# Optimization experiments

Measured on AMD Instinct MI355X. Metric: run time of the kernel, lower is better.

## Reference

```python
import jax, jax.numpy as jnp
import numpy as np


def _unfold(x, k, pad, stride):
    # torch.nn.functional.unfold: [B,C,H,W] -> [B, C*k*k, L]
    B, C, H, W = x.shape
    xp = jnp.pad(x, ((0, 0), (0, 0), (pad, pad), (pad, pad)))
    Ho = (H + 2 * pad - k) // stride + 1
    Wo = (W + 2 * pad - k) // stride + 1
    ih = stride * jnp.arange(Ho)[:, None] + jnp.arange(k)[None, :]  # [Ho,k]
    iw = stride * jnp.arange(Wo)[:, None] + jnp.arange(k)[None, :]  # [Wo,k]
    p = xp[:, :, ih][:, :, :, :, iw]          # [B,C,Ho,k,Wo,k]
    p = p.transpose(0, 1, 3, 5, 2, 4)          # [B,C,k,k,Ho,Wo]
    return p.reshape(B, C * k * k, Ho * Wo)


def _fold(cols, out_hw, k, pad, stride):
    # torch.nn.functional.fold (col2im, overlap-add)
    B, D, L = cols.shape
    C = D // (k * k)
    Ho = (out_hw[0] + 2 * pad - k) // stride + 1
    Wo = (out_hw[1] + 2 * pad - k) // stride + 1
    x = cols.reshape(B, C, k, k, Ho, Wo).transpose(0, 1, 2, 4, 3, 5)  # [B,C,k,Ho,k,Wo]
    ih = stride * jnp.arange(Ho)[None, :] + jnp.arange(k)[:, None]    # [k,Ho]
    iw = stride * jnp.arange(Wo)[None, :] + jnp.arange(k)[:, None]    # [k,Wo]
    out = jnp.zeros((B, C, out_hw[0] + 2 * pad, out_hw[1] + 2 * pad), cols.dtype)
    out = out.at[:, :, ih[:, :, None, None], iw[None, None, :, :]].add(x)
    return out[:, :, pad:pad + out_hw[0], pad:pad + out_hw[1]]


def _l2norm(x, axis):
    # torch F.normalize with eps=1e-12 (clamp_min on the norm)
    n = jnp.sqrt(jnp.sum(x * x, axis=axis, keepdims=True))
    return x / jnp.clip(n, 1e-12)


def _cubic(x):
    # PyTorch bicubic kernel, a=-0.75
    a = -0.75
    ax = jnp.abs(x)
    ax2 = ax * ax
    ax3 = ax2 * ax
    w1 = (a + 2.0) * ax3 - (a + 3.0) * ax2 + 1.0
    w2 = a * ax3 - 5.0 * a * ax2 + 8.0 * a * ax - 4.0 * a
    return jnp.where(ax <= 1.0, w1, jnp.where(ax < 2.0, w2, 0.0))


def _upsample1d_bicubic(x, axis, scale):
    # align_corners=False: src = (dst+0.5)/scale - 0.5, border-replicated 4-tap
    n = x.shape[axis]
    out = jnp.arange(n * scale, dtype=jnp.float32)
    src = (out + 0.5) / scale - 0.5
    f = jnp.floor(src)
    t = src - f
    offs = jnp.arange(-1, 3)
    idx = jnp.clip(f[:, None].astype(jnp.int32) + offs[None, :], 0, n - 1)   # [No,4]
    w = _cubic(t[:, None] - offs[None, :].astype(jnp.float32))               # [No,4]
    g = jnp.take(x, idx, axis=axis)  # inserts dims (No,4) at `axis`
    w_shape = [1] * g.ndim
    w_shape[axis] = idx.shape[0]
    w_shape[axis + 1] = 4
    return jnp.sum(g * w.reshape(w_shape), axis=axis + 1)


def _bicubic(R, scale):
    # R: [B, N_ref, N_lr] treated as a 1-channel image, upscale both axes
    R = _upsample1d_bicubic(R, 1, scale)
    return _upsample1d_bicubic(R, 2, scale)


def setup_inputs() -> dict:
    key = jax.random.key(0)
    ks = jax.random.split(key, 9)
    shapes = {
        'lrsr_lv1': (2, 256, 16, 16), 'lrsr_lv2': (2, 128, 32, 32), 'lrsr_lv3': (2, 64, 64, 64),
        'refsr_lv1': (2, 256, 16, 16), 'refsr_lv2': (2, 128, 32, 32), 'refsr_lv3': (2, 64, 64, 64),
        'ref_lv1': (2, 64, 256, 256), 'ref_lv2': (2, 128, 128, 128), 'ref_lv3': (2, 256, 64, 64),
    }
    return {name: jax.random.normal(k, shp, dtype=jnp.float32)
            for k, (name, shp) in zip(ks, shapes.items())}


def reference(lrsr_lv1, lrsr_lv2, lrsr_lv3, refsr_lv1, refsr_lv2, refsr_lv3, ref_lv1, ref_lv2, ref_lv3):
    # unfold + L2-normalize descriptors
    l3 = _l2norm(_unfold(lrsr_lv3, 3, 1, 1), 1)   # [B, D3, N3]
    l2 = _l2norm(_unfold(lrsr_lv2, 3, 1, 1), 1)
    l1 = _l2norm(_unfold(lrsr_lv1, 3, 1, 1), 1)
    r3 = _l2norm(jnp.swapaxes(_unfold(refsr_lv3, 3, 1, 1), 1, 2), 2)  # [B, N3, D3]
    r2 = _l2norm(jnp.swapaxes(_unfold(refsr_lv2, 3, 1, 1), 1, 2), 2)
    r1 = _l2norm(jnp.swapaxes(_unfold(refsr_lv1, 3, 1, 1), 1, 2), 2)
    # cosine correlation per scale
    R3 = jnp.einsum('bnd,bdm->bnm', r3, l3)   # [B, N3, N3]
    R2 = jnp.einsum('bnd,bdm->bnm', r2, l2)   # [B, N3/4, N3/4]
    R1 = jnp.einsum('bnd,bdm->bnm', r1, l1)   # [B, N3/16, N3/16]
    R = (R3 + _bicubic(R2, 4) + _bicubic(R1, 16)) / 3.0
    star = jnp.max(R, axis=1)                 # [B, N3]
    arg = jnp.argmax(R, axis=1)               # [B, N3]
    # retrieval gather on reference patches
    u3 = _unfold(ref_lv3, 3, 1, 1)
    u2 = _unfold(ref_lv2, 6, 2, 2)
    u1 = _unfold(ref_lv1, 12, 4, 4)
    gather = lambda u: jnp.take_along_axis(u, arg[:, None, :], axis=2)
    B = lrsr_lv3.shape[0]
    H, W = lrsr_lv3.shape[2], lrsr_lv3.shape[3]
    T_lv3 = _fold(gather(u3), (H, W), 3, 1, 1) / 9.0
    T_lv2 = _fold(gather(u2), (2 * H, 2 * W), 6, 2, 2) / 9.0
    T_lv1 = _fold(gather(u1), (4 * H, 4 * W), 12, 4, 4) / 9.0
    S_3 = star.reshape(B, 1, H, W)
    return (S_3, T_lv3, T_lv2, T_lv1)
```

## Files before the change

### kernel.cpp

```cpp
#include <hip/hip_runtime.h>
#include <cstdint>

#define DIVUP(a,b) (((a)+(b)-1)/(b))

typedef __attribute__((ext_vector_type(4))) float f32x4;
typedef __attribute__((ext_vector_type(8))) _Float16 half8;

__device__ __forceinline__ void gload_lds16(const void* g, void* l) {
  __builtin_amdgcn_global_load_lds(
      (const __attribute__((address_space(1))) void*)g,
      (__attribute__((address_space(3))) void*)l, 16, 0, 0);
}

__device__ __forceinline__ float cubicw(float x) {
  float ax = fabsf(x);
  float ax2 = ax * ax;
  float ax3 = ax2 * ax;
  if (ax <= 1.0f) return 1.25f * ax3 - 2.25f * ax2 + 1.0f;
  if (ax < 2.0f)  return -0.75f * ax3 + 3.75f * ax2 - 6.0f * ax + 3.0f;
  return 0.0f;
}

__global__ void sumsq_multi(const float* __restrict__ r3, const float* __restrict__ l3,
                            const float* __restrict__ r2, const float* __restrict__ l2,
                            const float* __restrict__ r1, const float* __restrict__ l1,
                            float* __restrict__ S) {
  int blk = blockIdx.x;
  const float* x; int C, HW, so, base;
  if (blk < 32)      { x = r3; C = 64;  HW = 4096; so = 0;     base = 0;  }
  else if (blk < 64) { x = l3; C = 64;  HW = 4096; so = 8192;  base = 32; }
  else if (blk < 72) { x = r2; C = 128; HW = 1024; so = 16384; base = 64; }
  else if (blk < 80) { x = l2; C = 128; HW = 1024; so = 18432; base = 72; }
  else if (blk < 82) { x = r1; C = 256; HW = 256;  so = 20480; base = 80; }
  else               { x = l1; C = 256; HW = 256;  so = 20992; base = 82; }
  int i = (blk - base) * 256 + threadIdx.x;
  if (i >= 2 * HW) return;
  int pix = i % HW, b = i / HW;
  const float* p = x + (size_t)b * C * HW + pix;
  float s = 0.f;
  for (int c = 0; c < C; ++c) { float v = p[(size_t)c * HW]; s += v * v; }
  S[so + i] = s;
}

__global__ void invnorm_multi(const float* __restrict__ S, float* __restrict__ invn) {
  int blk = blockIdx.x;
  int H, so, base;
  if (blk < 32)      { H = 64; so = 0;     base = 0;  }
  else if (blk < 64) { H = 64; so = 8192;  base = 32; }
  else if (blk < 72) { H = 32; so = 16384; base = 64; }
  else if (blk < 80) { H = 32; so = 18432; base = 72; }
  else if (blk < 82) { H = 16; so = 20480; base = 80; }
  else               { H = 16; so = 20992; base = 82; }
  int W = H;
  int i = (blk - base) * 256 + threadIdx.x;
  if (i >= 2 * H * W) return;
  int p = i % (H * W), b = i / (H * W);
  int ph = p / W, pw = p % W;
  const float* Sb = S + so + (size_t)b * H * W;
  float s = 0.f;
  for (int ki = 0; ki < 3; ++ki) {
    int y = ph + ki - 1;
    if (y < 0 || y >= H) continue;
    for (int kj = 0; kj < 3; ++kj) {
      int xx = pw + kj - 1;
      if (xx < 0 || xx >= W) continue;
      s += Sb[y * W + xx];
    }
  }
  float n = fmaxf(sqrtf(s), 1e-12f);
  invn[so + i] = 1.0f / n;
}

__global__ void desc_split_multi(const float* __restrict__ r3, const float* __restrict__ l3,
                                 const float* __restrict__ r2, const float* __restrict__ l2,
                                 _Float16* __restrict__ r3hi, _Float16* __restrict__ r3lo,
                                 _Float16* __restrict__ l3hi, _Float16* __restrict__ l3lo,
                                 _Float16* __restrict__ r2hi, _Float16* __restrict__ r2lo,
                                 _Float16* __restrict__ l2hi, _Float16* __restrict__ l2lo,
                                 const float* __restrict__ invn) {
  int blk = blockIdx.x;
  const float* x; _Float16* hi; _Float16* lo; int C, H, io, base;
  if (blk < 2048)      { x = r3; hi = r3hi; lo = r3lo; C = 64;  H = 64; io = 0;     base = 0; }
  else if (blk < 4096) { x = l3; hi = l3hi; lo = l3lo; C = 64;  H = 64; io = 8192;  base = 2048; }
  else if (blk < 5120) { x = r2; hi = r2hi; lo = r2lo; C = 128; H = 32; io = 16384; base = 4096; }
  else                 { x = l2; hi = l2hi; lo = l2lo; C = 128; H = 32; io = 18432; base = 5120; }
  int W = H, HW = H * W;
  int i = (blk - base) * 256 + threadIdx.x;
  if (i >= 2 * C * HW) return;
  int c = i % C;
  int p = (i / C) % HW;
  int b = i / (C * HW);
  int ph = p / W, pw = p % W;
  float s = invn[io + b * HW + p];
  size_t obase = ((size_t)b * HW + p) * (size_t)(C * 9) + (size_t)c * 9;
  const float* xb = x + (size_t)(b * C + c) * HW;
#pragma unroll
  for (int r = 0; r < 9; ++r) {
    int y = ph + r / 3 - 1, xx = pw + r % 3 - 1;
    float v = 0.f;
    if (y >= 0 && y < H && xx >= 0 && xx < W) v = xb[y * W + xx] * s;
    _Float16 h = (_Float16)v;
    float hf = (float)h;
    _Float16 l = (_Float16)((v - hf) * 4096.0f);
    hi[obase + r] = h;
    lo[obase + r] = l;
  }
}

__global__ void desc_l1_kernel(const float* __restrict__ x, float* __restrict__ out,
                               const float* __restrict__ invn) {
  const int C = 256, H = 16, W = 16, HW = 256, D = 2304, io = 20992;
  int i = blockIdx.x * 256 + threadIdx.x;
  if (i >= 2 * D * HW) return;
  int p = i % HW;
  int d = (i / HW) % D;
  int b = i / (HW * D);
  int c = d / 9, r = d % 9, ki = r / 3, kj = r % 3;
  int ph = p / W, pw = p % W;
  int y = ph + ki - 1, xx = pw + kj - 1;
  float v = 0.f;
  if (y >= 0 && y < H && xx >= 0 && xx < W) v = x[((size_t)(b * C + c) * H + y) * W + xx];
  out[i] = v * invn[io + b * HW + p];
}

__global__ void desc_r1_kernel(const float* __restrict__ x, float* __restrict__ out,
                               const float* __restrict__ invn) {
  const int C = 256, H = 16, W = 16, HW = 256, D = 2304, io = 20480;
  int i = blockIdx.x * 256 + threadIdx.x;
  if (i >= 2 * D * HW) return;
  int d = i % D;
  int p = (i / D) % HW;
  int b = i / (D * HW);
  int c = d / 9, r = d % 9, ki = r / 3, kj = r % 3;
  int ph = p / W, pw = p % W;
  int y = ph + ki - 1, xx = pw + kj - 1;
  float v = 0.f;
  if (y >= 0 && y < H && xx >= 0 && xx < W) v = x[((size_t)(b * C + c) * H + y) * W + xx];
  out[i] = v * invn[io + b * HW + p];
}

__global__ void upsample_multi(const float* __restrict__ R2, const float* __restrict__ R1,
                               float* __restrict__ up2, float* __restrict__ up1) {
  int blk = blockIdx.x;
  const float* Rin; float* out; int Nin, cols, base; float invscale;
  if (blk < 32768) { Rin = R2; out = up2; Nin = 1024; cols = 1024; invscale = 0.25f;   base = 0; }
  else             { Rin = R1; out = up1; Nin = 256;  cols = 256;  invscale = 0.0625f; base = 32768; }
  int i = (blk - base) * 256 + threadIdx.x;
  if (i >= 2 * 4096 * cols) return;
  int j = i % cols;
  int n = (i / cols) & 4095;
  int b = i / (cols * 4096);
  float src = (n + 0.5f) * invscale - 0.5f;
  float f = floorf(src);
  float tt = src - f;
  int fi = (int)f;
  const float* Rb = Rin + (size_t)b * Nin * cols;
  float s = 0.f;
#pragma unroll
  for (int tp = 0; tp < 4; ++tp) {
    int ii = min(max(fi + tp - 1, 0), Nin - 1);
    s += cubicw(tt - (float)(tp - 1)) * Rb[(size_t)ii * cols + j];
  }
  out[i] = s;
}

__global__ void init_multi(unsigned long long* __restrict__ R1z,
                           unsigned long long* __restrict__ pk) {
  int i = blockIdx.x * blockDim.x + threadIdx.x;
  if (i < 65536) R1z[i] = 0ull;
  else if (i < 65536 + 8192) pk[i - 65536] = 0ull;
}

__global__ __launch_bounds__(256)
void gemm64sk_kernel(const float* __restrict__ A, const float* __restrict__ B,
                     float* __restrict__ C, int M, int N, int K, int SK) {
  int zz = blockIdx.z;
  int b = zz / SK, kc = zz % SK;
  int kchunk = K / SK;
  int kbeg = kc * kchunk, kend = kbeg + kchunk;
  const float* Ab = A + (size_t)b * M * K;
  const float* Bb = B + (size_t)b * K * N;
  __shared__ float As[16][68];
  __shared__ float Bs[16][64];
  int row0 = blockIdx.y * 64;
  int col0 = blockIdx.x * 64;
  int t = threadIdx.x;
  int tx = t & 15, ty = t >> 4;
  float acc[4][4] = {};
  int la_r = t >> 2;
  int la_k = (t & 3) << 2;
  int lb_r = t >> 4;
  int lb_c = (t & 15) << 2;
  const float* Aptr = Ab + (size_t)(row0 + la_r) * K + la_k;
  const float* Bptr = Bb + (size_t)lb_r * N + col0 + lb_c;
  float4 av = *(const float4*)(Aptr + kbeg);
  float4 bv = *(const float4*)(Bptr + (size_t)kbeg * N);
  for (int k0 = kbeg; k0 < kend; k0 += 16) {
    __syncthreads();
    As[la_k + 0][la_r] = av.x;
    As[la_k + 1][la_r] = av.y;
    As[la_k + 2][la_r] = av.z;
    As[la_k + 3][la_r] = av.w;
    *(float4*)&Bs[lb_r][lb_c] = bv;
    __syncthreads();
    if (k0 + 16 < kend) {
      av = *(const float4*)(Aptr + k0 + 16);
      bv = *(const float4*)(Bptr + (size_t)(k0 + 16) * N);
    }
#pragma unroll
    for (int k = 0; k < 16; ++k) {
      float4 a = *(const float4*)&As[k][ty << 2];
      float4 bq = *(const float4*)&Bs[k][tx << 2];
      float av4[4] = {a.x, a.y, a.z, a.w};
      float bv4[4] = {bq.x, bq.y, bq.z, bq.w};
#pragma unroll
      for (int ii = 0; ii < 4; ++ii)
#pragma unroll
        for (int jj = 0; jj < 4; ++jj)
          acc[ii][jj] = fmaf(av4[ii], bv4[jj], acc[ii][jj]);
    }
  }
  float* Cb = C + (size_t)b * M * N;
#pragma unroll
  for (int ii = 0; ii < 4; ++ii)
#pragma unroll
    for (int jj = 0; jj < 4; ++jj)
      atomicAdd(&Cb[(size_t)(row0 + (ty << 2) + ii) * N + col0 + (tx << 2) + jj],
                acc[ii][jj]);
}

__global__ __launch_bounds__(256, 2)
void mfma_r2_kernel(const _Float16* __restrict__ Ahi, const _Float16* __restrict__ Alo,
                    const _Float16* __restrict__ Bhi, const _Float16* __restrict__ Blo,
                    float* __restrict__ Cout) {
  const int K = 1152;
  int bx = blockIdx.x, by = blockIdx.y, b = blockIdx.z;
  int row0 = by * 128;
  int col0 = bx * 128;
  int t = threadIdx.x;
  int lane = t & 63, wave = t >> 6;
  int wy = wave & 1, wx = wave >> 1;
  int quad = lane >> 4, lm = lane & 15;

  __shared__ _Float16 lds[2 * 4 * 4096];

  int off[2];
#pragma unroll
  for (int h = 0; h < 2; ++h) {
    int d = wave * 128 + h * 64 + lane;
    int line = d >> 3;
    int c3 = (d & 7) ^ (line & 7);
    int row = (line << 1) | (c3 >> 2);
    int c = c3 & 3;
    off[h] = row * (K * 2) + c * 16;
  }
  const char* pg[4];
  pg[0] = (const char*)Ahi + ((size_t)b * 1024 + row0) * (size_t)K * 2;
  pg[1] = (const char*)Alo + ((size_t)b * 1024 + row0) * (size_t)K * 2;
  pg[2] = (const char*)Bhi + ((size_t)b * 1024 + col0) * (size_t)K * 2;
  pg[3] = (const char*)Blo + ((size_t)b * 1024 + col0) * (size_t)K * 2;

  int ra[4], rb[4];
#pragma unroll
  for (int i = 0; i < 4; ++i) {
    int rowa = wy * 64 + i * 16 + lm;
    int la_ = rowa >> 1;
    ra[i] = la_ * 128 + (((((rowa & 1) << 2) | quad) ^ (la_ & 7)) << 4);
    int rowb = wx * 64 + i * 16 + lm;
    int lb_ = rowb >> 1;
    rb[i] = lb_ * 128 + (((((rowb & 1) << 2) | quad) ^ (lb_ & 7)) << 4);
  }

  f32x4 S1[4][4] = {};
  f32x4 S2[4][4] = {};

#pragma unroll
  for (int p = 0; p < 4; ++p) {
    char* lb_ = (char*)lds + p * 8192 + wave * 2048;
    gload_lds16(pg[p] + off[0], lb_);
    gload_lds16(pg[p] + off[1], lb_ + 1024);
  }
  __syncthreads();

  int buf = 0;
  for (int tki = 0; tki < 36; ++tki) {
    const char* lb = (const char*)lds + buf * 32768;
    half8 aH[4], aL[4], bH[4], bL[4];
#pragma unroll
    for (int i = 0; i < 4; ++i) {
      aH[i] = *(const half8*)(lb + ra[i]);
      aL[i] = *(const half8*)(lb + 8192 + ra[i]);
      bH[i] = *(const half8*)(lb + 16384 + rb[i]);
      bL[i] = *(const half8*)(lb + 24576 + rb[i]);
    }
    if (tki < 35) {
      int kbyte = (tki + 1) * 64;
#pragma unroll
      for (int p = 0; p < 4; ++p) {
        char* lw = (char*)lds + (buf ^ 1) * 32768 + p * 8192 + wave * 2048;
        gload_lds16(pg[p] + kbyte + off[0], lw);
        gload_lds16(pg[p] + kbyte + off[1], lw + 1024);
      }
    }
#pragma unroll
    for (int i = 0; i < 4; ++i)
#pragma unroll
      for (int j = 0; j < 4; ++j) {
        S1[i][j] = __builtin_amdgcn_mfma_f32_16x16x32_f16(aH[i], bH[j], S1[i][j], 0, 0, 0);
        S2[i][j] = __builtin_amdgcn_mfma_f32_16x16x32_f16(aH[i], bL[j], S2[i][j], 0, 0, 0);
        S2[i][j] = __builtin_amdgcn_mfma_f32_16x16x32_f16(aL[i], bH[j], S2[i][j], 0, 0, 0);
      }
    __syncthreads();
    buf ^= 1;
  }

  const float inv4096 = 1.0f / 4096.0f;
  float* Cb = Cout + (size_t)b * 1024 * 1024;
#pragma unroll
  for (int i = 0; i < 4; ++i)
#pragma unroll
    for (int j = 0; j < 4; ++j)
#pragma unroll
      for (int r = 0; r < 4; ++r) {
        int gn = row0 + wy * 64 + i * 16 + quad * 4 + r;
        int gm = col0 + wx * 64 + j * 16 + lm;
        Cb[(size_t)gn * 1024 + gm] = S1[i][j][r] + S2[i][j][r] * inv4096;
      }
}

__global__ __launch_bounds__(256, 2)
void mfma_fused_kernel(const _Float16* __restrict__ Ahi, const _Float16* __restrict__ Alo,
                       const _Float16* __restrict__ Bhi, const _Float16* __restrict__ Blo,
                       const float* __restrict__ up2, const float* __restrict__ up1,
                       unsigned long long* __restrict__ packed) {
  const int K = 576;
  int bid = (blockIdx.z * 32 + blockIdx.y) * 32 + blockIdx.x;
  int swz = (bid & 7) * 256 + (bid >> 3);
  int bx = swz & 31;
  int by = (swz >> 5) & 31;
  int b  = swz >> 10;

  int row0 = by * 128;
  int col0 = bx * 128;
  int t = threadIdx.x;
  int lane = t & 63, wave = t >> 6;
  int wy = wave & 1, wx = wave >> 1;
  int quad = lane >> 4, lm = lane & 15;

  __shared__ _Float16 lds[2 * 4 * 4096];

  int off[2];
#pragma unroll
  for (int h = 0; h < 2; ++h) {
    int d = wave * 128 + h * 64 + lane;
    int line = d >> 3;
    int c3 = (d & 7) ^ (line & 7);
    int row = (line << 1) | (c3 >> 2);
    int c = c3 & 3;
    off[h] = row * (K * 2) + c * 16;
  }
  const char* pg[4];
  pg[0] = (const char*)Ahi + ((size_t)b * 4096 + row0) * (size_t)K * 2;
  pg[1] = (const char*)Alo + ((size_t)b * 4096 + row0) * (size_t)K * 2;
  pg[2] = (const char*)Bhi + ((size_t)b * 4096 + col0) * (size_t)K * 2;
  pg[3] = (const char*)Blo + ((size_t)b * 4096 + col0) * (size_t)K * 2;

  int ra[4], rb[4];
#pragma unroll
  for (int i = 0; i < 4; ++i) {
    int rowa = wy * 64 + i * 16 + lm;
    int la_ = rowa >> 1;
    ra[i] = la_ * 128 + (((((rowa & 1) << 2) | quad) ^ (la_ & 7)) << 4);
    int rowb = wx * 64 + i * 16 + lm;
    int lb_ = rowb >> 1;
    rb[i] = lb_ * 128 + (((((rowb & 1) << 2) | quad) ^ (lb_ & 7)) << 4);
  }

  f32x4 S1[4][4] = {};
  f32x4 S2[4][4] = {};

#pragma unroll
  for (int p = 0; p < 4; ++p) {
    char* lb_ = (char*)lds + p * 8192 + wave * 2048;
    gload_lds16(pg[p] + off[0], lb_);
    gload_lds16(pg[p] + off[1], lb_ + 1024);
  }
  __syncthreads();

  int buf = 0;
  for (int t18 = 0; t18 < 18; ++t18) {
    const char* lb = (const char*)lds + buf * 32768;
    half8 aH[4], aL[4], bH[4], bL[4];
#pragma unroll
    for (int i = 0; i < 4; ++i) {
      aH[i] = *(const half8*)(lb + ra[i]);
      aL[i] = *(const half8*)(lb + 8192 + ra[i]);
      bH[i] = *(const half8*)(lb + 16384 + rb[i]);
      bL[i] = *(const half8*)(lb + 24576 + rb[i]);
    }
    if (t18 < 17) {
      int kbyte = (t18 + 1) * 64;
#pragma unroll
      for (int p = 0; p < 4; ++p) {
        char* lw = (char*)lds + (buf ^ 1) * 32768 + p * 8192 + wave * 2048;
        gload_lds16(pg[p] + kbyte + off[0], lw);
        gload_lds16(pg[p] + kbyte + off[1], lw + 1024);
      }
    }
#pragma unroll
    for (int i = 0; i < 4; ++i)
#pragma unroll
      for (int j = 0; j < 4; ++j) {
        S1[i][j] = __builtin_amdgcn_mfma_f32_16x16x32_f16(aH[i], bH[j], S1[i][j], 0, 0, 0);
        S2[i][j] = __builtin_amdgcn_mfma_f32_16x16x32_f16(aH[i], bL[j], S2[i][j], 0, 0, 0);
        S2[i][j] = __builtin_amdgcn_mfma_f32_16x16x32_f16(aL[i], bH[j], S2[i][j], 0, 0, 0);
      }
    __syncthreads();
    buf ^= 1;
  }

  const float inv4096 = 1.0f / 4096.0f;
  const float* u2b = up2 + (size_t)b * 4096 * 1024;
  const float* u1b = up1 + (size_t)b * 4096 * 256;
#pragma unroll
  for (int j = 0; j < 4; ++j) {
    int gm = col0 + wx * 64 + j * 16 + lm;
    float src2 = (gm + 0.5f) * 0.25f - 0.5f;
    float f2 = floorf(src2); float t2 = src2 - f2; int i2 = (int)f2;
    int idx2[4]; float w2[4];
#pragma unroll
    for (int tp = 0; tp < 4; ++tp) {
      idx2[tp] = min(max(i2 + tp - 1, 0), 1023);
      w2[tp] = cubicw(t2 - (float)(tp - 1));
    }
    float src1 = (gm + 0.5f) * 0.0625f - 0.5f;
    float f1 = floorf(src1); float t1 = src1 - f1; int i1 = (int)f1;
    int idx1[4]; float w1[4];
#pragma unroll
    for (int tp = 0; tp < 4; ++tp) {
      idx1[tp] = min(max(i1 + tp - 1, 0), 255);
      w1[tp] = cubicw(t1 - (float)(tp - 1));
    }
    unsigned long long best = 0ull;
#pragma unroll
    for (int i = 0; i < 4; ++i) {
#pragma unroll
      for (int r = 0; r < 4; ++r) {
        int gn = row0 + wy * 64 + i * 16 + quad * 4 + r;
        float v = S1[i][j][r] + S2[i][j][r] * inv4096;
        const float* r2row = u2b + (size_t)gn * 1024;
        const float* r1row = u1b + (size_t)gn * 256;
        v += w2[0] * r2row[idx2[0]] + w2[1] * r2row[idx2[1]]
           + w2[2] * r2row[idx2[2]] + w2[3] * r2row[idx2[3]];
        v += w1[0] * r1row[idx1[0]] + w1[1] * r1row[idx1[1]]
           + w1[2] * r1row[idx1[2]] + w1[3] * r1row[idx1[3]];
        v *= (1.0f / 3.0f);
        unsigned int fb = __float_as_uint(v);
        unsigned int key = (fb & 0x80000000u) ? ~fb : (fb | 0x80000000u);
        unsigned long long pk = ((unsigned long long)key << 32)
                              | (unsigned long long)(0xFFFFFFFFu - (unsigned)gn);
        best = best > pk ? best : pk;
      }
    }
    unsigned long long o;
    o = __shfl_xor(best, 16); best = best > o ? best : o;
    o = __shfl_xor(best, 32); best = best > o ? best : o;
    if (lane < 16) atomicMax(&packed[(size_t)b * 4096 + gm], best);
  }
}

__global__ void finalize_kernel(const unsigned long long* __restrict__ packed,
                                float* __restrict__ s3_out, int* __restrict__ arg, int total) {
  int i = blockIdx.x * blockDim.x + threadIdx.x;
  if (i >= total) return;
  unsigned long long pk = packed[i];
  unsigned int key = (unsigned int)(pk >> 32);
  unsigned int fb = (key & 0x80000000u) ? (key ^ 0x80000000u) : ~key;
  s3_out[i] = __uint_as_float(fb);
  arg[i] = (int)(0xFFFFFFFFu - (unsigned int)(pk & 0xFFFFFFFFull));
}

__global__ __launch_bounds__(256)
void transpose_multi(const float* __restrict__ ref3, const float* __restrict__ ref2,
                     const float* __restrict__ ref1, float* __restrict__ o3,
                     float* __restrict__ o2, float* __restrict__ o1) {
  __shared__ float tile[32][33];
  int blk = blockIdx.x;
  const float* in; float* out; int R, S, gx, gy, base;
  if (blk < 2048)      { in = ref3; out = o3; R = 256; S = 4096;  gx = 128;  gy = 8; base = 0; }
  else if (blk < 6144) { in = ref2; out = o2; R = 128; S = 16384; gx = 512;  gy = 4; base = 2048; }
  else                 { in = ref1; out = o1; R = 64;  S = 65536; gx = 2048; gy = 2; base = 6144; }
  int local = blk - base;
  int pb = gx * gy;
  int b = local / pb;
  int rem = local % pb;
  int r0 = (rem / gx) * 32;
  int s0 = (rem % gx) * 32;
  int tx = threadIdx.x & 31, ty = threadIdx.x >> 5;
  const float* ib = in + (size_t)b * R * S;
  float* ob = out + (size_t)b * R * S;
#pragma unroll
  for (int k = 0; k < 4; ++k)
    tile[ty + 8 * k][tx] = ib[(size_t)(r0 + ty + 8 * k) * S + s0 + tx];
  __syncthreads();
#pragma unroll
  for (int k = 0; k < 4; ++k)
    ob[(size_t)(s0 + ty + 8 * k) * R + r0 + tx] = tile[tx][ty + 8 * k];
}

template<int KK, int SS, int PP, int CL2, int WL2>
__device__ __forceinline__ void foldT_body(const float* __restrict__ refT,
                                           const int* __restrict__ arg,
                                           float* __restrict__ outCF,
                                           float* lds, int bx, int h, int b) {
  const int C = 1 << CL2, W = 1 << WL2;
  const int NK = (C / 4) / 16;
  int tid = threadIdx.x;
  int pl = tid >> 4, c4g = tid & 15;
  int w0 = bx * 16;
  int w = w0 + pl;
  int y = h + PP, x = w + PP;
  int ho_lo = (y - KK + 1) > 0 ? (y - KK + 1 + SS - 1) / SS : 0;
  int ho_hi = min(63, y / SS);
  int wo_lo = (x - KK + 1) > 0 ? (x - KK + 1 + SS - 1) / SS : 0;
  int wo_hi = min(63, x / SS);
  const int* argb = arg + b * 4096;
  const f32x4* refb4 = (const f32x4*)(refT + ((size_t)b << (2 * WL2 + CL2)));
  f32x4 acc[NK] = {};
  for (int ho = ho_lo; ho <= ho_hi; ++ho) {
    int ki = y - SS * ho;
    for (int wo = wo_lo; wo <= wo_hi; ++wo) {
      int kj = x - SS * wo;
      int q = argb[(ho << 6) + wo];
      int qh = q >> 6, qw = q & 63;
      int ry = SS * qh + ki - PP;
      int rx = SS * qw + kj - PP;
      if (ry >= 0 && ry < W && rx >= 0 && rx < W) {
        const f32x4* pb4 = refb4 + (((size_t)(ry << WL2) + rx) << (CL2 - 2));
#pragma unroll
        for (int k = 0; k < NK; ++k) acc[k] += pb4[c4g + k * 16];
      }
    }
  }
#pragma unroll
  for (int k = 0; k < NK; ++k) {
    int c4 = c4g + k * 16;
#pragma unroll
    for (int j = 0; j < 4; ++j)
      lds[(4 * c4 + j) * 17 + pl] = acc[k][j] * (1.0f / 9.0f);
  }
  __syncthreads();
  size_t ob = ((size_t)(b * C)) << (2 * WL2);
  for (int idx = tid; idx < C * 16; idx += 256) {
    int c = idx >> 4, j = idx & 15;
    outCF[ob + ((size_t)c << (2 * WL2)) + (h << WL2) + w0 + j] = lds[c * 17 + j];
  }
}

__global__ __launch_bounds__(256)
void foldT_all(const float* __restrict__ refT3, const float* __restrict__ refT2,
               const float* __restrict__ refT1, const int* __restrict__ arg,
               float* __restrict__ T3, float* __restrict__ T2, float* __restrict__ T1) {
  __shared__ float lds[256 * 17];
  int blk = blockIdx.x;
  if (blk < 512) {
    int local = blk;
    foldT_body<3, 1, 1, 8, 6>(refT3, arg, T3, lds, local & 3, (local >> 2) & 63, local >> 8);
  } else if (blk < 2560) {
    int local = blk - 512;
    foldT_body<6, 2, 2, 7, 7>(refT2, arg, T2, lds, local & 7, (local >> 3) & 127, local >> 10);
  } else {
    int local = blk - 2560;
    foldT_body<12, 4, 4, 6, 8>(refT1, arg, T1, lds, local & 15, (local >> 4) & 255, local >> 12);
  }
}

extern "C" void kernel_launch(void* const* d_in, const int* in_sizes, int n_in,
                              void* d_out, int out_size, void* d_ws, size_t ws_size,
                              hipStream_t stream) {
  const float* lrsr1 = (const float*)d_in[0];
  const float* lrsr2 = (const float*)d_in[1];
  const float* lrsr3 = (const float*)d_in[2];
  const float* refsr1 = (const float*)d_in[3];
  const float* refsr2 = (const float*)d_in[4];
  const float* refsr3 = (const float*)d_in[5];
  const float* ref1 = (const float*)d_in[6];
  const float* ref2 = (const float*)d_in[7];
  const float* ref3 = (const float*)d_in[8];
  float* out = (float*)d_out;
  float* ws = (float*)d_ws;

  const int B = 2;
  size_t off_planes = 0;
  size_t off_pl2 = off_planes + (size_t)B * 4096 * 576 * 2;
  size_t off_r1n = off_pl2 + (size_t)B * 1024 * 1152 * 2;
  size_t off_l1n = off_r1n + (size_t)B * 256 * 2304;
  size_t off_R2  = off_l1n + (size_t)B * 2304 * 256;
  size_t off_R1  = off_R2  + (size_t)B * 1024 * 1024;
  size_t off_up2 = off_R1  + (size_t)B * 256 * 256;
  size_t off_up1 = off_up2 + (size_t)B * 4096 * 1024;
  size_t off_S   = off_up1 + (size_t)B * 4096 * 256;
  size_t off_invn= off_S   + 21504;
  size_t off_pk  = off_invn+ 21504;
  size_t off_arg = off_pk  + (size_t)B * 4096 * 2;

  const size_t PLANE3 = (size_t)B * 4096 * 576;
  _Float16* r3hi = (_Float16*)(ws + off_planes);
  _Float16* r3lo = r3hi + PLANE3;
  _Float16* l3hi = r3lo + PLANE3;
  _Float16* l3lo = l3hi + PLANE3;
  const size_t PLANE2 = (size_t)B * 1024 * 1152;
  _Float16* r2hi = (_Float16*)(ws + off_pl2);
  _Float16* r2lo = r2hi + PLANE2;
  _Float16* l2hi = r2lo + PLANE2;
  _Float16* l2lo = l2hi + PLANE2;

  unsigned long long* pk = (unsigned long long*)(ws + off_pk);
  int* argp = (int*)(ws + off_arg);

  init_multi<<<288, 256, 0, stream>>>((unsigned long long*)(ws + off_R1), pk);
  sumsq_multi<<<84, 256, 0, stream>>>(refsr3, lrsr3, refsr2, lrsr2, refsr1, lrsr1,
                                      ws + off_S);
  invnorm_multi<<<84, 256, 0, stream>>>(ws + off_S, ws + off_invn);
  desc_split_multi<<<6144, 256, 0, stream>>>(refsr3, lrsr3, refsr2, lrsr2,
                                             r3hi, r3lo, l3hi, l3lo,
                                             r2hi, r2lo, l2hi, l2lo,
                                             ws + off_invn);
  desc_l1_kernel<<<4608, 256, 0, stream>>>(lrsr1, ws + off_l1n, ws + off_invn);
  desc_r1_kernel<<<4608, 256, 0, stream>>>(refsr1, ws + off_r1n, ws + off_invn);
  {
    dim3 g(8, 8, B);
    mfma_r2_kernel<<<g, 256, 0, stream>>>(r2hi, r2lo, l2hi, l2lo, ws + off_R2);
  }
  {
    dim3 g(256 / 64, 256 / 64, B * 8);
    gemm64sk_kernel<<<g, 256, 0, stream>>>(ws + off_r1n, ws + off_l1n, ws + off_R1,
                                           256, 256, 2304, 8);
  }
  upsample_multi<<<40960, 256, 0, stream>>>(ws + off_R2, ws + off_R1,
                                            ws + off_up2, ws + off_up1);
  {
    dim3 g(4096 / 128, 4096 / 128, B);
    mfma_fused_kernel<<<g, 256, 0, stream>>>(r3hi, r3lo, l3hi, l3lo,
                                             ws + off_up2, ws + off_up1, pk);
  }
  finalize_kernel<<<DIVUP(B * 4096, 256), 256, 0, stream>>>(pk, out, argp, B * 4096);

  float* refT3 = ws + off_planes;
  float* refT2 = refT3 + (size_t)2 * 256 * 4096;
  float* refT1 = ws + off_up2;
  transpose_multi<<<14336, 256, 0, stream>>>(ref3, ref2, ref1, refT3, refT2, refT1);

  float* T3 = out + 8192;
  float* T2 = T3 + (size_t)B * 256 * 64 * 64;
  float* T1 = T2 + (size_t)B * 128 * 128 * 128;
  foldT_all<<<10752, 256, 0, stream>>>(refT3, refT2, refT1, argp, T3, T2, T1);
}
```

Baseline: 639.5 us.

## Split-K the R2 MFMA GEMM and channel reductions, merge level-1 descriptor kernels

The R2 correlation GEMM is split into two K halves, doubling the block count, and the partial results are combined with float atomics into a buffer that is now zeroed in the init kernel. The sum-of-squares reduction is split across 8 channel slices per block, also combined with atomics. The two level-1 descriptor kernels are merged into one launch. The aim is more parallelism on small grids and fewer launches, at the cost of extra zeroing traffic, atomic contention and nondeterministic float summation order.

```diff
diff --git a/kernel.cpp b/kernel.cpp
--- a/kernel.cpp
+++ b/kernel.cpp
@@ -26,20 +26,23 @@
                             const float* __restrict__ r1, const float* __restrict__ l1,
                             float* __restrict__ S) {
   int blk = blockIdx.x;
+  int slice = blk & 7;
+  int jb = blk >> 3;
   const float* x; int C, HW, so, base;
-  if (blk < 32)      { x = r3; C = 64;  HW = 4096; so = 0;     base = 0;  }
-  else if (blk < 64) { x = l3; C = 64;  HW = 4096; so = 8192;  base = 32; }
-  else if (blk < 72) { x = r2; C = 128; HW = 1024; so = 16384; base = 64; }
-  else if (blk < 80) { x = l2; C = 128; HW = 1024; so = 18432; base = 72; }
-  else if (blk < 82) { x = r1; C = 256; HW = 256;  so = 20480; base = 80; }
-  else               { x = l1; C = 256; HW = 256;  so = 20992; base = 82; }
-  int i = (blk - base) * 256 + threadIdx.x;
+  if (jb < 32)      { x = r3; C = 64;  HW = 4096; so = 0;     base = 0;  }
+  else if (jb < 64) { x = l3; C = 64;  HW = 4096; so = 8192;  base = 32; }
+  else if (jb < 72) { x = r2; C = 128; HW = 1024; so = 16384; base = 64; }
+  else if (jb < 80) { x = l2; C = 128; HW = 1024; so = 18432; base = 72; }
+  else if (jb < 82) { x = r1; C = 256; HW = 256;  so = 20480; base = 80; }
+  else              { x = l1; C = 256; HW = 256;  so = 20992; base = 82; }
+  int i = (jb - base) * 256 + threadIdx.x;
   if (i >= 2 * HW) return;
   int pix = i % HW, b = i / HW;
+  int c0 = slice * (C >> 3), c1 = c0 + (C >> 3);
   const float* p = x + (size_t)b * C * HW + pix;
   float s = 0.f;
-  for (int c = 0; c < C; ++c) { float v = p[(size_t)c * HW]; s += v * v; }
-  S[so + i] = s;
+  for (int c = c0; c < c1; ++c) { float v = p[(size_t)c * HW]; s += v * v; }
+  atomicAdd(&S[so + i], s);
 }
 
 __global__ void invnorm_multi(const float* __restrict__ S, float* __restrict__ invn) {
@@ -107,30 +110,20 @@
   }
 }
 
-__global__ void desc_l1_kernel(const float* __restrict__ x, float* __restrict__ out,
+__global__ void desc_f32_multi(const float* __restrict__ lin, const float* __restrict__ rin,
+                               float* __restrict__ l1n, float* __restrict__ r1n,
                                const float* __restrict__ invn) {
-  const int C = 256, H = 16, W = 16, HW = 256, D = 2304, io = 20992;
-  int i = blockIdx.x * 256 + threadIdx.x;
+  const int C = 256, H = 16, W = 16, HW = 256, D = 2304;
+  int blk = blockIdx.x;
+  bool rlay = blk >= 4608;
+  const float* x = rlay ? rin : lin;
+  float* out = rlay ? r1n : l1n;
+  int io = rlay ? 20480 : 20992;
+  int i = (rlay ? blk - 4608 : blk) * 256 + threadIdx.x;
   if (i >= 2 * D * HW) return;
-  int p = i % HW;
-  int d = (i / HW) % D;
-  int b = i / (HW * D);
-  int c = d / 9, r = d % 9, ki = r / 3, kj = r % 3;
-  int ph = p / W, pw = p % W;
-  int y = ph + ki - 1, xx = pw + kj - 1;
-  float v = 0.f;
-  if (y >= 0 && y < H && xx >= 0 && xx < W) v = x[((size_t)(b * C + c) * H + y) * W + xx];
-  out[i] = v * invn[io + b * HW + p];
-}
-
-__global__ void desc_r1_kernel(const float* __restrict__ x, float* __restrict__ out,
-                               const float* __restrict__ invn) {
-  const int C = 256, H = 16, W = 16, HW = 256, D = 2304, io = 20480;
-  int i = blockIdx.x * 256 + threadIdx.x;
-  if (i >= 2 * D * HW) return;
-  int d = i % D;
-  int p = (i / D) % HW;
-  int b = i / (D * HW);
+  int p, d, b;
+  if (rlay) { d = i % D; p = (i / D) % HW; b = i / (D * HW); }
+  else      { p = i % HW; d = (i / HW) % D; b = i / (HW * D); }
   int c = d / 9, r = d % 9, ki = r / 3, kj = r % 3;
   int ph = p / W, pw = p % W;
   int y = ph + ki - 1, xx = pw + kj - 1;
@@ -165,10 +158,14 @@
 }
 
 __global__ void init_multi(unsigned long long* __restrict__ R1z,
-                           unsigned long long* __restrict__ pk) {
+                           unsigned long long* __restrict__ pk,
+                           unsigned long long* __restrict__ R2z,
+                           unsigned long long* __restrict__ Sz) {
   int i = blockIdx.x * blockDim.x + threadIdx.x;
   if (i < 65536) R1z[i] = 0ull;
   else if (i < 65536 + 8192) pk[i - 65536] = 0ull;
+  else if (i < 65536 + 8192 + 1048576) R2z[i - 65536 - 8192] = 0ull;
+  else if (i < 65536 + 8192 + 1048576 + 21504) Sz[i - 65536 - 8192 - 1048576] = 0ull;
 }
 
 __global__ __launch_bounds__(256)
@@ -234,7 +231,10 @@
                     const _Float16* __restrict__ Bhi, const _Float16* __restrict__ Blo,
                     float* __restrict__ Cout) {
   const int K = 1152;
-  int bx = blockIdx.x, by = blockIdx.y, b = blockIdx.z;
+  int bx = blockIdx.x, by = blockIdx.y;
+  int zz = blockIdx.z;
+  int b = zz >> 1, kc = zz & 1;
+  int kbyte0 = kc * 1152;
   int row0 = by * 128;
   int col0 = bx * 128;
   int t = threadIdx.x;
@@ -277,13 +277,13 @@
 #pragma unroll
   for (int p = 0; p < 4; ++p) {
     char* lb_ = (char*)lds + p * 8192 + wave * 2048;
-    gload_lds16(pg[p] + off[0], lb_);
-    gload_lds16(pg[p] + off[1], lb_ + 1024);
+    gload_lds16(pg[p] + kbyte0 + off[0], lb_);
+    gload_lds16(pg[p] + kbyte0 + off[1], lb_ + 1024);
   }
   __syncthreads();
 
   int buf = 0;
-  for (int tki = 0; tki < 36; ++tki) {
+  for (int tki = 0; tki < 18; ++tki) {
     const char* lb = (const char*)lds + buf * 32768;
     half8 aH[4], aL[4], bH[4], bL[4];
 #pragma unroll
@@ -293,8 +293,8 @@
       bH[i] = *(const half8*)(lb + 16384 + rb[i]);
       bL[i] = *(const half8*)(lb + 24576 + rb[i]);
     }
-    if (tki < 35) {
-      int kbyte = (tki + 1) * 64;
+    if (tki < 17) {
+      int kbyte = kbyte0 + (tki + 1) * 64;
 #pragma unroll
       for (int p = 0; p < 4; ++p) {
         char* lw = (char*)lds + (buf ^ 1) * 32768 + p * 8192 + wave * 2048;
@@ -324,7 +324,7 @@
       for (int r = 0; r < 4; ++r) {
         int gn = row0 + wy * 64 + i * 16 + quad * 4 + r;
         int gm = col0 + wx * 64 + j * 16 + lm;
-        Cb[(size_t)gn * 1024 + gm] = S1[i][j][r] + S2[i][j][r] * inv4096;
+        atomicAdd(&Cb[(size_t)gn * 1024 + gm], S1[i][j][r] + S2[i][j][r] * inv4096);
       }
 }
 
@@ -618,18 +618,20 @@
   unsigned long long* pk = (unsigned long long*)(ws + off_pk);
   int* argp = (int*)(ws + off_arg);
 
-  init_multi<<<288, 256, 0, stream>>>((unsigned long long*)(ws + off_R1), pk);
-  sumsq_multi<<<84, 256, 0, stream>>>(refsr3, lrsr3, refsr2, lrsr2, refsr1, lrsr1,
-                                      ws + off_S);
+  init_multi<<<DIVUP(65536 + 8192 + 1048576 + 21504, 256), 256, 0, stream>>>(
+      (unsigned long long*)(ws + off_R1), pk,
+      (unsigned long long*)(ws + off_R2), (unsigned long long*)(ws + off_S));
+  sumsq_multi<<<84 * 8, 256, 0, stream>>>(refsr3, lrsr3, refsr2, lrsr2, refsr1, lrsr1,
+                                          ws + off_S);
   invnorm_multi<<<84, 256, 0, stream>>>(ws + off_S, ws + off_invn);
   desc_split_multi<<<6144, 256, 0, stream>>>(refsr3, lrsr3, refsr2, lrsr2,
                                              r3hi, r3lo, l3hi, l3lo,
                                              r2hi, r2lo, l2hi, l2lo,
                                              ws + off_invn);
-  desc_l1_kernel<<<4608, 256, 0, stream>>>(lrsr1, ws + off_l1n, ws + off_invn);
-  desc_r1_kernel<<<4608, 256, 0, stream>>>(refsr1, ws + off_r1n, ws + off_invn);
+  desc_f32_multi<<<9216, 256, 0, stream>>>(lrsr1, refsr1, ws + off_l1n, ws + off_r1n,
+                                           ws + off_invn);
   {
-    dim3 g(8, 8, B);
+    dim3 g(8, 8, B * 2);
     mfma_r2_kernel<<<g, 256, 0, stream>>>(r2hi, r2lo, l2hi, l2lo, ws + off_R2);
   }
   {
```

Measured after the change: 555.2 us. -13.2%, faster.
